# Kernel tuning notes

Hardware: AMD Instinct MI355X
Metric: run time of the kernel (lower is better)

The kernel has to match this reference:

```python
import jax, jax.numpy as jnp
import numpy as np

NODE_DIM = 8
IN_EDGE_DIM = 4
OUT_EDGE_DIM = 4
HID = 16
N_NODES = 100000
N_EDGES = 3200000
LN_EPS = 1e-5


def _layer_norm(h, gamma, beta):
    mu = jnp.mean(h, axis=-1, keepdims=True)
    var = jnp.mean(jnp.square(h - mu), axis=-1, keepdims=True)
    return (h - mu) * jax.lax.rsqrt(var + LN_EPS) * gamma + beta


def setup_inputs() -> dict:
    key = jax.random.key(0)
    ks = jax.random.split(key, 12)
    in_dim = NODE_DIM * 2 + IN_EDGE_DIM  # 20
    x = jax.random.normal(ks[0], (N_NODES, NODE_DIM), dtype=jnp.float32)
    edge_index = jax.random.randint(ks[1], (2, N_EDGES), 0, N_NODES, dtype=jnp.int64)
    edge_attr = jax.random.normal(ks[2], (N_EDGES, IN_EDGE_DIM), dtype=jnp.float32)
    # MLP params (Kaiming-uniform-ish scaling like torch defaults)
    def lin(k, fan_in, fan_out):
        lim = 1.0 / np.sqrt(fan_in)
        kw, kb = jax.random.split(k)
        W = jax.random.uniform(kw, (fan_in, fan_out), minval=-lim, maxval=lim, dtype=jnp.float32)
        b = jax.random.uniform(kb, (fan_out,), minval=-lim, maxval=lim, dtype=jnp.float32)
        return W, b
    W1, b1 = lin(ks[3], in_dim, HID)
    W2, b2 = lin(ks[4], HID, HID)
    W3, b3 = lin(ks[5], HID, OUT_EDGE_DIM)
    g1 = jnp.ones((HID,), jnp.float32); be1 = jnp.zeros((HID,), jnp.float32)
    g2 = jnp.ones((HID,), jnp.float32); be2 = jnp.zeros((HID,), jnp.float32)
    return {"x": x, "edge_index": edge_index, "edge_attr": edge_attr,
            "W1": W1, "b1": b1, "g1": g1, "be1": be1,
            "W2": W2, "b2": b2, "g2": g2, "be2": be2,
            "W3": W3, "b3": b3}


def reference(x, edge_index, edge_attr, W1, b1, g1, be1, W2, b2, g2, be2, W3, b3):
    frm = edge_index[0]
    to = edge_index[1]
    # gather node features for both endpoints, concat with edge features: [E, 2*node_dim+in_edge_dim]
    inpt = jnp.concatenate([x[frm], x[to], edge_attr.astype(jnp.float32)], axis=1)
    h = _layer_norm(jax.nn.relu(inpt @ W1 + b1), g1, be1)
    h = _layer_norm(jax.nn.relu(h @ W2 + b2), g2, be2)
    return h @ W3 + b3  # [E, out_edge_dim]
```

## Files before the change

### kernel.cpp

```cpp
#include <hip/hip_runtime.h>
#include <stdint.h>


using u16 = unsigned short;
using u32 = uint32_t;

__device__ __forceinline__ float bf2f(u16 u) { return __uint_as_float(((u32)u) << 16); }
__device__ __forceinline__ float bflo(u32 u) { return __uint_as_float(u << 16); }
__device__ __forceinline__ float bfhi(u32 u) { return __uint_as_float(u & 0xFFFF0000u); }
__device__ __forceinline__ u32 f2bf(float f) {
    u32 u = __float_as_uint(f);
    return (u + 0x7FFFu + ((u >> 16) & 1u)) >> 16;
}
__device__ __forceinline__ float ldw(const void* p, int i, bool bf) {
    return bf ? bf2f(((const u16*)p)[i]) : ((const float*)p)[i];
}

#define WB_W1 0
#define WB_W2 320
#define WB_W3 576
#define WB_B1 640
#define WB_G1 656
#define WB_BE1 672
#define WB_B2 688
#define WB_G2 704
#define WB_BE2 720
#define WB_B3 736

__device__ __forceinline__ void relu_ln16_2(float* h0, float* h1,
                                            const float* __restrict__ g,
                                            const float* __restrict__ be) {
    float s0 = 0.f, s1 = 0.f;
#pragma unroll
    for (int j = 0; j < 16; j++) {
        h0[j] = fmaxf(h0[j], 0.f); s0 += h0[j];
        h1[j] = fmaxf(h1[j], 0.f); s1 += h1[j];
    }
    float mu0 = s0 * 0.0625f, mu1 = s1 * 0.0625f;
    float v0 = 0.f, v1 = 0.f;
#pragma unroll
    for (int j = 0; j < 16; j++) {
        float d0 = h0[j] - mu0; v0 = fmaf(d0, d0, v0);
        float d1 = h1[j] - mu1; v1 = fmaf(d1, d1, v1);
    }
    float r0 = rsqrtf(v0 * 0.0625f + 1e-5f);
    float r1 = rsqrtf(v1 * 0.0625f + 1e-5f);
#pragma unroll
    for (int j = 0; j < 16; j++) {
        h0[j] = (h0[j] - mu0) * r0 * g[j] + be[j];
        h1[j] = (h1[j] - mu1) * r1 * g[j] + be[j];
    }
}

__global__ __launch_bounds__(256)
void probe_convert(const int* __restrict__ ei, int n_pairs,
                   const void* W1, const void* b1, const void* g1, const void* be1,
                   const void* W2, const void* b2, const void* g2, const void* be2,
                   const void* W3, const void* b3,
                   int* __restrict__ flags, float* __restrict__ wb) {
    bool bf = (((const u32*)g1)[0] == 0x3F803F80u);
    __shared__ int s;
    if (threadIdx.x == 0) s = 0;
    __syncthreads();
    int limit = n_pairs < 2048 ? n_pairs : 2048;
    int found = 0;
    for (int i = threadIdx.x; i < limit; i += blockDim.x)
        if (ei[2 * i + 1] != 0) found = 1;
    if (found) s = 1;
    __syncthreads();
    if (threadIdx.x == 0) { flags[0] = s; flags[1] = bf ? 1 : 0; }
    int t = threadIdx.x;
    for (int i = t; i < 320; i += 256) wb[WB_W1 + i] = ldw(W1, i, bf);
    for (int i = t; i < 256; i += 256) wb[WB_W2 + i] = ldw(W2, i, bf);
    if (t < 64) wb[WB_W3 + t] = ldw(W3, t, bf);
    if (t < 16) {
        wb[WB_B1 + t] = ldw(b1, t, bf);   wb[WB_G1 + t] = ldw(g1, t, bf);
        wb[WB_BE1 + t] = ldw(be1, t, bf); wb[WB_B2 + t] = ldw(b2, t, bf);
        wb[WB_G2 + t] = ldw(g2, t, bf);   wb[WB_BE2 + t] = ldw(be2, t, bf);
        if (t < 4) wb[WB_B3 + t] = ldw(b3, t, bf);
    }
}

__global__ __launch_bounds__(256)
void edge_mlp(const void* __restrict__ x, const int* __restrict__ ei,
              const void* __restrict__ ea, const float* __restrict__ wb,
              const int* __restrict__ flags, void* __restrict__ out, int n_edges) {
    const bool idx32 = flags[0] != 0;
    const bool bf = flags[1] != 0;

    int e0 = blockIdx.x * 512 + threadIdx.x;
    int e1 = e0 + 256;
    bool v0 = e0 < n_edges, v1 = e1 < n_edges;
    int ec0 = v0 ? e0 : 0, ec1 = v1 ? e1 : 0;

    int f0, f1, t0, t1;
    if (idx32) {
        f0 = ei[ec0]; f1 = ei[ec1];
        t0 = ei[n_edges + ec0]; t1 = ei[n_edges + ec1];
    } else {
        f0 = ei[2 * (size_t)ec0]; f1 = ei[2 * (size_t)ec1];
        t0 = ei[2 * ((size_t)n_edges + ec0)]; t1 = ei[2 * ((size_t)n_edges + ec1)];
    }

    float xv0[16], xv1[16];
    if (bf) {
        uint4 a0 = ((const uint4*)x)[f0], c0 = ((const uint4*)x)[t0];
        uint4 a1 = ((const uint4*)x)[f1], c1 = ((const uint4*)x)[t1];
        xv0[0] = bflo(a0.x); xv0[1] = bfhi(a0.x); xv0[2] = bflo(a0.y); xv0[3] = bfhi(a0.y);
        xv0[4] = bflo(a0.z); xv0[5] = bfhi(a0.z); xv0[6] = bflo(a0.w); xv0[7] = bfhi(a0.w);
        xv0[8] = bflo(c0.x); xv0[9] = bfhi(c0.x); xv0[10] = bflo(c0.y); xv0[11] = bfhi(c0.y);
        xv0[12] = bflo(c0.z); xv0[13] = bfhi(c0.z); xv0[14] = bflo(c0.w); xv0[15] = bfhi(c0.w);
        xv1[0] = bflo(a1.x); xv1[1] = bfhi(a1.x); xv1[2] = bflo(a1.y); xv1[3] = bfhi(a1.y);
        xv1[4] = bflo(a1.z); xv1[5] = bfhi(a1.z); xv1[6] = bflo(a1.w); xv1[7] = bfhi(a1.w);
        xv1[8] = bflo(c1.x); xv1[9] = bfhi(c1.x); xv1[10] = bflo(c1.y); xv1[11] = bfhi(c1.y);
        xv1[12] = bflo(c1.z); xv1[13] = bfhi(c1.z); xv1[14] = bflo(c1.w); xv1[15] = bfhi(c1.w);
    } else {
        const float4* xp = (const float4*)x;
        float4 a0 = xp[2 * f0], b0 = xp[2 * f0 + 1];
        float4 c0 = xp[2 * t0], d0 = xp[2 * t0 + 1];
        float4 a1 = xp[2 * f1], b1v = xp[2 * f1 + 1];
        float4 c1 = xp[2 * t1], d1 = xp[2 * t1 + 1];
        xv0[0] = a0.x; xv0[1] = a0.y; xv0[2] = a0.z; xv0[3] = a0.w;
        xv0[4] = b0.x; xv0[5] = b0.y; xv0[6] = b0.z; xv0[7] = b0.w;
        xv0[8] = c0.x; xv0[9] = c0.y; xv0[10] = c0.z; xv0[11] = c0.w;
        xv0[12] = d0.x; xv0[13] = d0.y; xv0[14] = d0.z; xv0[15] = d0.w;
        xv1[0] = a1.x; xv1[1] = a1.y; xv1[2] = a1.z; xv1[3] = a1.w;
        xv1[4] = b1v.x; xv1[5] = b1v.y; xv1[6] = b1v.z; xv1[7] = b1v.w;
        xv1[8] = c1.x; xv1[9] = c1.y; xv1[10] = c1.z; xv1[11] = c1.w;
        xv1[12] = d1.x; xv1[13] = d1.y; xv1[14] = d1.z; xv1[15] = d1.w;
    }

    float ev0[4], ev1[4];
    if (bf) {
        uint2 r0 = ((const uint2*)ea)[ec0], r1 = ((const uint2*)ea)[ec1];
        ev0[0] = bflo(r0.x); ev0[1] = bfhi(r0.x); ev0[2] = bflo(r0.y); ev0[3] = bfhi(r0.y);
        ev1[0] = bflo(r1.x); ev1[1] = bfhi(r1.x); ev1[2] = bflo(r1.y); ev1[3] = bfhi(r1.y);
    } else {
        float4 r0 = ((const float4*)ea)[ec0], r1 = ((const float4*)ea)[ec1];
        ev0[0] = r0.x; ev0[1] = r0.y; ev0[2] = r0.z; ev0[3] = r0.w;
        ev1[0] = r1.x; ev1[1] = r1.y; ev1[2] = r1.z; ev1[3] = r1.w;
    }

    float h0[16], h1[16];
#pragma unroll
    for (int j = 0; j < 16; j++) { h0[j] = wb[WB_B1 + j]; h1[j] = h0[j]; }
#pragma unroll
    for (int k = 0; k < 16; k++) {
        float a0 = xv0[k], a1 = xv1[k];
#pragma unroll
        for (int j = 0; j < 16; j++) {
            float w = wb[WB_W1 + k * 16 + j];
            h0[j] = fmaf(a0, w, h0[j]);
            h1[j] = fmaf(a1, w, h1[j]);
        }
    }
#pragma unroll
    for (int k = 0; k < 4; k++) {
        float a0 = ev0[k], a1 = ev1[k];
#pragma unroll
        for (int j = 0; j < 16; j++) {
            float w = wb[WB_W1 + (16 + k) * 16 + j];
            h0[j] = fmaf(a0, w, h0[j]);
            h1[j] = fmaf(a1, w, h1[j]);
        }
    }

    relu_ln16_2(h0, h1, wb + WB_G1, wb + WB_BE1);

    float a0[16], a1[16];
#pragma unroll
    for (int j = 0; j < 16; j++) { a0[j] = wb[WB_B2 + j]; a1[j] = a0[j]; }
#pragma unroll
    for (int k = 0; k < 16; k++) {
        float hk0 = h0[k], hk1 = h1[k];
#pragma unroll
        for (int j = 0; j < 16; j++) {
            float w = wb[WB_W2 + k * 16 + j];
            a0[j] = fmaf(hk0, w, a0[j]);
            a1[j] = fmaf(hk1, w, a1[j]);
        }
    }

    relu_ln16_2(a0, a1, wb + WB_G2, wb + WB_BE2);

    float o0[4], o1[4];
#pragma unroll
    for (int j = 0; j < 4; j++) { o0[j] = wb[WB_B3 + j]; o1[j] = o0[j]; }
#pragma unroll
    for (int k = 0; k < 16; k++) {
        float hk0 = a0[k], hk1 = a1[k];
#pragma unroll
        for (int j = 0; j < 4; j++) {
            float w = wb[WB_W3 + k * 4 + j];
            o0[j] = fmaf(hk0, w, o0[j]);
            o1[j] = fmaf(hk1, w, o1[j]);
        }
    }

    if (bf) {
        uint2 p0, p1;
        p0.x = f2bf(o0[0]) | (f2bf(o0[1]) << 16);
        p0.y = f2bf(o0[2]) | (f2bf(o0[3]) << 16);
        p1.x = f2bf(o1[0]) | (f2bf(o1[1]) << 16);
        p1.y = f2bf(o1[2]) | (f2bf(o1[3]) << 16);
        if (v0) ((uint2*)out)[e0] = p0;
        if (v1) ((uint2*)out)[e1] = p1;
    } else {
        if (v0) ((float4*)out)[e0] = make_float4(o0[0], o0[1], o0[2], o0[3]);
        if (v1) ((float4*)out)[e1] = make_float4(o1[0], o1[1], o1[2], o1[3]);
    }
}

extern "C" void kernel_launch(void* const* d_in, const int* in_sizes, int n_in,
                              void* d_out, int out_size, void* d_ws, size_t ws_size,
                              hipStream_t stream) {
    const void* x  = d_in[0];
    const int* ei  = (const int*)d_in[1];
    const void* ea = d_in[2];

    int n_edges = in_sizes[1] / 2;

    int* flags = (int*)d_ws;
    float* wb = (float*)((char*)d_ws + 64);

    probe_convert<<<1, 256, 0, stream>>>(ei, n_edges,
                                         d_in[3], d_in[4], d_in[5], d_in[6],
                                         d_in[7], d_in[8], d_in[9], d_in[10],
                                         d_in[11], d_in[12], flags, wb);

    int eblocks = (n_edges + 511) / 512;
    edge_mlp<<<eblocks, 256, 0, stream>>>(x, ei, ea, wb, flags, d_out, n_edges);
}
```

Measured before the change: 200.0 us.

## Fold LayerNorm affine into next layer weights and stage weights in LDS

Folds the LayerNorm gamma/beta of each hidden layer into the following linear layer's weights and bias in the setup kernel, leaving only normalize-with-FMA in the edge kernel. Variance is computed in a single pass from sum and sum of squares, and the weights are copied into shared memory per block instead of being read from global memory. The single-pass variance is less numerically robust, and the shared-memory staging adds a barrier and LDS reads in place of scalar global or constant loads.

```diff
diff --git a/kernel.cpp b/kernel.cpp
--- a/kernel.cpp
+++ b/kernel.cpp
@@ -17,40 +17,12 @@
 }
 
 #define WB_W1 0
-#define WB_W2 320
-#define WB_W3 576
-#define WB_B1 640
-#define WB_G1 656
-#define WB_BE1 672
-#define WB_B2 688
-#define WB_G2 704
-#define WB_BE2 720
-#define WB_B3 736
-
-__device__ __forceinline__ void relu_ln16_2(float* h0, float* h1,
-                                            const float* __restrict__ g,
-                                            const float* __restrict__ be) {
-    float s0 = 0.f, s1 = 0.f;
-#pragma unroll
-    for (int j = 0; j < 16; j++) {
-        h0[j] = fmaxf(h0[j], 0.f); s0 += h0[j];
-        h1[j] = fmaxf(h1[j], 0.f); s1 += h1[j];
-    }
-    float mu0 = s0 * 0.0625f, mu1 = s1 * 0.0625f;
-    float v0 = 0.f, v1 = 0.f;
-#pragma unroll
-    for (int j = 0; j < 16; j++) {
-        float d0 = h0[j] - mu0; v0 = fmaf(d0, d0, v0);
-        float d1 = h1[j] - mu1; v1 = fmaf(d1, d1, v1);
-    }
-    float r0 = rsqrtf(v0 * 0.0625f + 1e-5f);
-    float r1 = rsqrtf(v1 * 0.0625f + 1e-5f);
-#pragma unroll
-    for (int j = 0; j < 16; j++) {
-        h0[j] = (h0[j] - mu0) * r0 * g[j] + be[j];
-        h1[j] = (h1[j] - mu1) * r1 * g[j] + be[j];
-    }
-}
+#define WB_B1 320
+#define WB_W2 336
+#define WB_B2 592
+#define WB_W3 608
+#define WB_B3 672
+#define WB_TOT 704
 
 __global__ __launch_bounds__(256)
 void probe_convert(const int* __restrict__ ei, int n_pairs,
@@ -69,15 +41,47 @@
     if (found) s = 1;
     __syncthreads();
     if (threadIdx.x == 0) { flags[0] = s; flags[1] = bf ? 1 : 0; }
+
     int t = threadIdx.x;
     for (int i = t; i < 320; i += 256) wb[WB_W1 + i] = ldw(W1, i, bf);
-    for (int i = t; i < 256; i += 256) wb[WB_W2 + i] = ldw(W2, i, bf);
-    if (t < 64) wb[WB_W3 + t] = ldw(W3, t, bf);
+    if (t < 16) wb[WB_B1 + t] = ldw(b1, t, bf);
+    {
+        int k = t >> 4;
+        wb[WB_W2 + t] = ldw(g1, k, bf) * ldw(W2, t, bf);
+    }
     if (t < 16) {
-        wb[WB_B1 + t] = ldw(b1, t, bf);   wb[WB_G1 + t] = ldw(g1, t, bf);
-        wb[WB_BE1 + t] = ldw(be1, t, bf); wb[WB_B2 + t] = ldw(b2, t, bf);
-        wb[WB_G2 + t] = ldw(g2, t, bf);   wb[WB_BE2 + t] = ldw(be2, t, bf);
-        if (t < 4) wb[WB_B3 + t] = ldw(b3, t, bf);
+        float acc = ldw(b2, t, bf);
+        for (int k = 0; k < 16; k++) acc = fmaf(ldw(be1, k, bf), ldw(W2, k * 16 + t, bf), acc);
+        wb[WB_B2 + t] = acc;
+    }
+    if (t < 64) {
+        int k = t >> 2;
+        wb[WB_W3 + t] = ldw(g2, k, bf) * ldw(W3, t, bf);
+    }
+    if (t < 4) {
+        float acc = ldw(b3, t, bf);
+        for (int k = 0; k < 16; k++) acc = fmaf(ldw(be2, k, bf), ldw(W3, k * 4 + t, bf), acc);
+        wb[WB_B3 + t] = acc;
+    }
+    if (t >= 676 - 672 && t < 704 - 672) wb[672 + t] = 0.f;
+}
+
+__device__ __forceinline__ void relu_ln16_nf(float* h0, float* h1) {
+    float s0 = 0.f, s1 = 0.f, q0 = 0.f, q1 = 0.f;
+#pragma unroll
+    for (int j = 0; j < 16; j++) {
+        h0[j] = fmaxf(h0[j], 0.f); s0 += h0[j]; q0 = fmaf(h0[j], h0[j], q0);
+        h1[j] = fmaxf(h1[j], 0.f); s1 += h1[j]; q1 = fmaf(h1[j], h1[j], q1);
+    }
+    float mu0 = s0 * 0.0625f, mu1 = s1 * 0.0625f;
+    float var0 = fmaf(-mu0, mu0, q0 * 0.0625f);
+    float var1 = fmaf(-mu1, mu1, q1 * 0.0625f);
+    float r0 = rsqrtf(var0 + 1e-5f), r1 = rsqrtf(var1 + 1e-5f);
+    float n0 = -mu0 * r0, n1 = -mu1 * r1;
+#pragma unroll
+    for (int j = 0; j < 16; j++) {
+        h0[j] = fmaf(h0[j], r0, n0);
+        h1[j] = fmaf(h1[j], r1, n1);
     }
 }
 
@@ -85,6 +89,11 @@
 void edge_mlp(const void* __restrict__ x, const int* __restrict__ ei,
               const void* __restrict__ ea, const float* __restrict__ wb,
               const int* __restrict__ flags, void* __restrict__ out, int n_edges) {
+    __shared__ float4 swv[WB_TOT / 4];
+    const float* sw = (const float*)swv;
+    for (int i = threadIdx.x; i < WB_TOT / 4; i += 256) swv[i] = ((const float4*)wb)[i];
+    __syncthreads();
+
     const bool idx32 = flags[0] != 0;
     const bool bf = flags[1] != 0;
 
@@ -102,98 +111,83 @@
         t0 = ei[2 * ((size_t)n_edges + ec0)]; t1 = ei[2 * ((size_t)n_edges + ec1)];
     }
 
-    float xv0[16], xv1[16];
+    float in0[20], in1[20];
     if (bf) {
         uint4 a0 = ((const uint4*)x)[f0], c0 = ((const uint4*)x)[t0];
         uint4 a1 = ((const uint4*)x)[f1], c1 = ((const uint4*)x)[t1];
-        xv0[0] = bflo(a0.x); xv0[1] = bfhi(a0.x); xv0[2] = bflo(a0.y); xv0[3] = bfhi(a0.y);
-        xv0[4] = bflo(a0.z); xv0[5] = bfhi(a0.z); xv0[6] = bflo(a0.w); xv0[7] = bfhi(a0.w);
-        xv0[8] = bflo(c0.x); xv0[9] = bfhi(c0.x); xv0[10] = bflo(c0.y); xv0[11] = bfhi(c0.y);
-        xv0[12] = bflo(c0.z); xv0[13] = bfhi(c0.z); xv0[14] = bflo(c0.w); xv0[15] = bfhi(c0.w);
-        xv1[0] = bflo(a1.x); xv1[1] = bfhi(a1.x); xv1[2] = bflo(a1.y); xv1[3] = bfhi(a1.y);
-        xv1[4] = bflo(a1.z); xv1[5] = bfhi(a1.z); xv1[6] = bflo(a1.w); xv1[7] = bfhi(a1.w);
-        xv1[8] = bflo(c1.x); xv1[9] = bfhi(c1.x); xv1[10] = bflo(c1.y); xv1[11] = bfhi(c1.y);
-        xv1[12] = bflo(c1.z); xv1[13] = bfhi(c1.z); xv1[14] = bflo(c1.w); xv1[15] = bfhi(c1.w);
+        uint2 r0 = ((const uint2*)ea)[ec0], r1 = ((const uint2*)ea)[ec1];
+        in0[0] = bflo(a0.x); in0[1] = bfhi(a0.x); in0[2] = bflo(a0.y); in0[3] = bfhi(a0.y);
+        in0[4] = bflo(a0.z); in0[5] = bfhi(a0.z); in0[6] = bflo(a0.w); in0[7] = bfhi(a0.w);
+        in0[8] = bflo(c0.x); in0[9] = bfhi(c0.x); in0[10] = bflo(c0.y); in0[11] = bfhi(c0.y);
+        in0[12] = bflo(c0.z); in0[13] = bfhi(c0.z); in0[14] = bflo(c0.w); in0[15] = bfhi(c0.w);
+        in0[16] = bflo(r0.x); in0[17] = bfhi(r0.x); in0[18] = bflo(r0.y); in0[19] = bfhi(r0.y);
+        in1[0] = bflo(a1.x); in1[1] = bfhi(a1.x); in1[2] = bflo(a1.y); in1[3] = bfhi(a1.y);
+        in1[4] = bflo(a1.z); in1[5] = bfhi(a1.z); in1[6] = bflo(a1.w); in1[7] = bfhi(a1.w);
+        in1[8] = bflo(c1.x); in1[9] = bfhi(c1.x); in1[10] = bflo(c1.y); in1[11] = bfhi(c1.y);
+        in1[12] = bflo(c1.z); in1[13] = bfhi(c1.z); in1[14] = bflo(c1.w); in1[15] = bfhi(c1.w);
+        in1[16] = bflo(r1.x); in1[17] = bfhi(r1.x); in1[18] = bflo(r1.y); in1[19] = bfhi(r1.y);
     } else {
         const float4* xp = (const float4*)x;
         float4 a0 = xp[2 * f0], b0 = xp[2 * f0 + 1];
         float4 c0 = xp[2 * t0], d0 = xp[2 * t0 + 1];
         float4 a1 = xp[2 * f1], b1v = xp[2 * f1 + 1];
         float4 c1 = xp[2 * t1], d1 = xp[2 * t1 + 1];
-        xv0[0] = a0.x; xv0[1] = a0.y; xv0[2] = a0.z; xv0[3] = a0.w;
-        xv0[4] = b0.x; xv0[5] = b0.y; xv0[6] = b0.z; xv0[7] = b0.w;
-        xv0[8] = c0.x; xv0[9] = c0.y; xv0[10] = c0.z; xv0[11] = c0.w;
-        xv0[12] = d0.x; xv0[13] = d0.y; xv0[14] = d0.z; xv0[15] = d0.w;
-        xv1[0] = a1.x; xv1[1] = a1.y; xv1[2] = a1.z; xv1[3] = a1.w;
-        xv1[4] = b1v.x; xv1[5] = b1v.y; xv1[6] = b1v.z; xv1[7] = b1v.w;
-        xv1[8] = c1.x; xv1[9] = c1.y; xv1[10] = c1.z; xv1[11] = c1.w;
-        xv1[12] = d1.x; xv1[13] = d1.y; xv1[14] = d1.z; xv1[15] = d1.w;
-    }
-
-    float ev0[4], ev1[4];
-    if (bf) {
-        uint2 r0 = ((const uint2*)ea)[ec0], r1 = ((const uint2*)ea)[ec1];
-        ev0[0] = bflo(r0.x); ev0[1] = bfhi(r0.x); ev0[2] = bflo(r0.y); ev0[3] = bfhi(r0.y);
-        ev1[0] = bflo(r1.x); ev1[1] = bfhi(r1.x); ev1[2] = bflo(r1.y); ev1[3] = bfhi(r1.y);
-    } else {
         float4 r0 = ((const float4*)ea)[ec0], r1 = ((const float4*)ea)[ec1];
-        ev0[0] = r0.x; ev0[1] = r0.y; ev0[2] = r0.z; ev0[3] = r0.w;
-        ev1[0] = r1.x; ev1[1] = r1.y; ev1[2] = r1.z; ev1[3] = r1.w;
+        in0[0] = a0.x; in0[1] = a0.y; in0[2] = a0.z; in0[3] = a0.w;
+        in0[4] = b0.x; in0[5] = b0.y; in0[6] = b0.z; in0[7] = b0.w;
+        in0[8] = c0.x; in0[9] = c0.y; in0[10] = c0.z; in0[11] = c0.w;
+        in0[12] = d0.x; in0[13] = d0.y; in0[14] = d0.z; in0[15] = d0.w;
+        in0[16] = r0.x; in0[17] = r0.y; in0[18] = r0.z; in0[19] = r0.w;
+        in1[0] = a1.x; in1[1] = a1.y; in1[2] = a1.z; in1[3] = a1.w;
+        in1[4] = b1v.x; in1[5] = b1v.y; in1[6] = b1v.z; in1[7] = b1v.w;
+        in1[8] = c1.x; in1[9] = c1.y; in1[10] = c1.z; in1[11] = c1.w;
+        in1[12] = d1.x; in1[13] = d1.y; in1[14] = d1.z; in1[15] = d1.w;
+        in1[16] = r1.x; in1[17] = r1.y; in1[18] = r1.z; in1[19] = r1.w;
     }
 
     float h0[16], h1[16];
 #pragma unroll
-    for (int j = 0; j < 16; j++) { h0[j] = wb[WB_B1 + j]; h1[j] = h0[j]; }
-#pragma unroll
-    for (int k = 0; k < 16; k++) {
-        float a0 = xv0[k], a1 = xv1[k];
+    for (int j = 0; j < 16; j++) { h0[j] = sw[WB_B1 + j]; h1[j] = h0[j]; }
+#pragma unroll
+    for (int k = 0; k < 20; k++) {
+        float a0 = in0[k], a1 = in1[k];
 #pragma unroll
         for (int j = 0; j < 16; j++) {
-            float w = wb[WB_W1 + k * 16 + j];
+            float w = sw[WB_W1 + k * 16 + j];
             h0[j] = fmaf(a0, w, h0[j]);
             h1[j] = fmaf(a1, w, h1[j]);
         }
     }
-#pragma unroll
-    for (int k = 0; k < 4; k++) {
-        float a0 = ev0[k], a1 = ev1[k];
+
+    relu_ln16_nf(h0, h1);
+
+    float a0v[16], a1v[16];
+#pragma unroll
+    for (int j = 0; j < 16; j++) { a0v[j] = sw[WB_B2 + j]; a1v[j] = a0v[j]; }
+#pragma unroll
+    for (int k = 0; k < 16; k++) {
+        float z0 = h0[k], z1 = h1[k];
 #pragma unroll
         for (int j = 0; j < 16; j++) {
-            float w = wb[WB_W1 + (16 + k) * 16 + j];
-            h0[j] = fmaf(a0, w, h0[j]);
-            h1[j] = fmaf(a1, w, h1[j]);
+            float w = sw[WB_W2 + k * 16 + j];
+            a0v[j] = fmaf(z0, w, a0v[j]);
+            a1v[j] = fmaf(z1, w, a1v[j]);
         }
     }
 
-    relu_ln16_2(h0, h1, wb + WB_G1, wb + WB_BE1);
-
-    float a0[16], a1[16];
-#pragma unroll
-    for (int j = 0; j < 16; j++) { a0[j] = wb[WB_B2 + j]; a1[j] = a0[j]; }
+    relu_ln16_nf(a0v, a1v);
+
+    float o0[4], o1[4];
+#pragma unroll
+    for (int j = 0; j < 4; j++) { o0[j] = sw[WB_B3 + j]; o1[j] = o0[j]; }
 #pragma unroll
     for (int k = 0; k < 16; k++) {
-        float hk0 = h0[k], hk1 = h1[k];
-#pragma unroll
-        for (int j = 0; j < 16; j++) {
-            float w = wb[WB_W2 + k * 16 + j];
-            a0[j] = fmaf(hk0, w, a0[j]);
-            a1[j] = fmaf(hk1, w, a1[j]);
-        }
-    }
-
-    relu_ln16_2(a0, a1, wb + WB_G2, wb + WB_BE2);
-
-    float o0[4], o1[4];
-#pragma unroll
-    for (int j = 0; j < 4; j++) { o0[j] = wb[WB_B3 + j]; o1[j] = o0[j]; }
-#pragma unroll
-    for (int k = 0; k < 16; k++) {
-        float hk0 = a0[k], hk1 = a1[k];
+        float z0 = a0v[k], z1 = a1v[k];
 #pragma unroll
         for (int j = 0; j < 4; j++) {
-            float w = wb[WB_W3 + k * 4 + j];
-            o0[j] = fmaf(hk0, w, o0[j]);
-            o1[j] = fmaf(hk1, w, o1[j]);
+            float w = sw[WB_W3 + k * 4 + j];
+            o0[j] = fmaf(z0, w, o0[j]);
+            o1[j] = fmaf(z1, w, o1[j]);
         }
     }
 
```

After: 196.1 us. No clear change (-1.9%).
